# Performance work log

Hardware: AMD Instinct MI355X
Metric: run time of the kernel (lower is better)

## Reference

```python
import jax, jax.numpy as jnp
import numpy as np

N_NODES = 100000

def sage_conv(x, edge_index, Wl, bl, Wr):
    # PyG SAGEConv: out = lin_l(mean_agg(x_src -> dst)) + lin_r(x)
    src, dst = edge_index[0], edge_index[1]
    msgs = x[src]                                   # [E, F] gather
    sums = jax.ops.segment_sum(msgs, dst, num_segments=N_NODES)   # [N, F]
    cnt = jax.ops.segment_sum(jnp.ones((edge_index.shape[1],), x.dtype), dst,
                              num_segments=N_NODES)               # [N]
    mean = sums / jnp.maximum(cnt, 1.0)[:, None]
    return mean @ Wl + bl + x @ Wr


def setup_inputs() -> dict:
    key = jax.random.key(0)
    ks = jax.random.split(key, 12)
    in_dim, hid = 32, 64
    x = jax.random.normal(ks[0], (N_NODES, in_dim), dtype=jnp.float32)
    edge_index = jax.random.randint(ks[1], (2, 3200000), 0, N_NODES)
    edge_pairs = jax.random.randint(ks[2], (1000000, 2), 0, N_NODES)
    def lin(k, fi, fo):
        bound = 1.0 / np.sqrt(fi)
        return jax.random.uniform(k, (fi, fo), jnp.float32, -bound, bound)
    params = {
        'Wl1': lin(ks[3], in_dim, hid), 'bl1': jnp.zeros((hid,), jnp.float32),
        'Wr1': lin(ks[4], in_dim, hid),
        'Wl2': lin(ks[5], hid, hid),    'bl2': jnp.zeros((hid,), jnp.float32),
        'Wr2': lin(ks[6], hid, hid),
        'Wh':  lin(ks[7], 2 * hid, 1),  'bh': jnp.zeros((1,), jnp.float32),
    }
    return dict(x=x, edge_index=edge_index, edge_pairs=edge_pairs, **params)


def reference(x, edge_index, edge_pairs, Wl1, bl1, Wr1, Wl2, bl2, Wr2, Wh, bh):
    h = jax.nn.relu(sage_conv(x, edge_index, Wl1, bl1, Wr1))
    h = jax.nn.relu(sage_conv(h, edge_index, Wl2, bl2, Wr2))
    src = h[edge_pairs[:, 0]]
    dst = h[edge_pairs[:, 1]]
    edge_repr = jnp.concatenate([src, dst], axis=1)   # [P, 2*hid]
    logits = (edge_repr @ Wh + bh)[:, 0]              # [P]
    return logits
```

## Files before the change

### kernel.cpp

```cpp
#include <hip/hip_runtime.h>

typedef unsigned int uint;
typedef unsigned short ushort;
typedef __attribute__((ext_vector_type(8))) short bf16x8;
typedef __attribute__((ext_vector_type(4))) float f32x4;

#define N_NODES 100000
#define N_EDGES 3200000
#define N_PAIRS 1000000
#define N_TILES (N_NODES / 16)

#define BUCK_SHIFT 8
#define BUCK_NODES 256
#define NBUCK ((N_NODES + BUCK_NODES - 1) / BUCK_NODES)
#define CAP 8704
#define CH 8192
#define NCHB ((N_EDGES + CH - 1) / CH)

__device__ __forceinline__ float bf_lo(uint u) { return __uint_as_float(u << 16); }
__device__ __forceinline__ float bf_hi(uint u) { return __uint_as_float(u & 0xFFFF0000u); }
__device__ __forceinline__ ushort f2bf(float f) {
  uint u = __float_as_uint(f);
  return (ushort)((u + 0x7FFF + ((u >> 16) & 1)) >> 16);
}
__device__ __forceinline__ uint pack2bf(float lo, float hi) {
  return (uint)f2bf(lo) | ((uint)f2bf(hi) << 16);
}


__global__ void __launch_bounds__(256) k_prep(
    const float* __restrict__ x,
    const float* __restrict__ Wl1, const float* __restrict__ Wr1,
    const float* __restrict__ Wl2, const float* __restrict__ Wr2,
    ushort* __restrict__ xb, ushort* __restrict__ W1T, ushort* __restrict__ W2T,
    int* __restrict__ woff)
{
  int t = blockIdx.x * blockDim.x + threadIdx.x;
  if (t < N_NODES * 32) xb[t] = f2bf(x[t]);
  if (t < 4096) {
    int col = t >> 6, f = t & 63;
    float w = (f < 32) ? Wl1[f * 64 + col] : Wr1[(f - 32) * 64 + col];
    W1T[col * 64 + f] = f2bf(w);
  }
  if (t < 8192) {
    int col = t >> 7, f = t & 127;
    float w = (f < 64) ? Wl2[f * 64 + col] : Wr2[(f - 64) * 64 + col];
    W2T[col * 128 + f] = f2bf(w);
  }
  if (t < NBUCK) woff[t] = t * CAP;
}


__global__ void __launch_bounds__(256) k_binning(
    const int* __restrict__ src, const int* __restrict__ dst,
    int* __restrict__ woff, int* __restrict__ bucket_data)
{
  __shared__ int hist[NBUCK];
  __shared__ int rbase[NBUCK];
  __shared__ int roff[NBUCK];
  int t = threadIdx.x;
  int lo = blockIdx.x * CH;
  int hi = lo + CH; if (hi > N_EDGES) hi = N_EDGES;
  for (int i = t; i < NBUCK; i += 256) { hist[i] = 0; roff[i] = 0; }
  __syncthreads();
  for (int e = lo + t; e < hi; e += 256) atomicAdd(&hist[dst[e] >> BUCK_SHIFT], 1);
  __syncthreads();
  for (int i = t; i < NBUCK; i += 256)
    rbase[i] = hist[i] ? atomicAdd(&woff[i], hist[i]) : 0;
  __syncthreads();
  for (int e = lo + t; e < hi; e += 256) {
    int d = dst[e];
    int b = d >> BUCK_SHIFT;
    int r = atomicAdd(&roff[b], 1);
    int pos = rbase[b] + r;
    if (pos < (b + 1) * CAP)
      bucket_data[pos] = (src[e] << BUCK_SHIFT) | (d & (BUCK_NODES - 1));
  }
}


__global__ void __launch_bounds__(512) k_bucket_csr(
    const int* __restrict__ woff, const int* __restrict__ bucket_data,
    int* __restrict__ csr, int* __restrict__ row_beg, int* __restrict__ row_end)
{
  __shared__ int hist[BUCK_NODES];
  __shared__ int sc[BUCK_NODES];
  __shared__ int offs[BUCK_NODES];
  int b = blockIdx.x;
  int t = threadIdx.x;
  int base = b * CAP;
  int cnt = woff[b] - base;
  const int* bd = bucket_data + base;
  if (t < BUCK_NODES) hist[t] = 0;
  __syncthreads();
  for (int i = t; i < cnt; i += 512) atomicAdd(&hist[bd[i] & (BUCK_NODES - 1)], 1);
  __syncthreads();
  if (t < BUCK_NODES) sc[t] = hist[t];
  __syncthreads();
  for (int off = 1; off < BUCK_NODES; off <<= 1) {
    int u = 0;
    if (t < BUCK_NODES && t >= off) u = sc[t - off];
    __syncthreads();
    if (t < BUCK_NODES) sc[t] += u;
    __syncthreads();
  }
  if (t < BUCK_NODES) {
    int start = base + sc[t] - hist[t];
    offs[t] = start;
    int node = b * BUCK_NODES + t;
    if (node < N_NODES) { row_beg[node] = start; row_end[node] = start + hist[t]; }
  }
  __syncthreads();
  for (int i = t; i < cnt; i += 512) {
    int pv = bd[i];
    int pos = atomicAdd(&offs[pv & (BUCK_NODES - 1)], 1);
    csr[pos] = pv >> BUCK_SHIFT;
  }
}


__global__ void __launch_bounds__(256) k_gather1(
    const uint4* __restrict__ xb4, const int* __restrict__ row_beg,
    const int* __restrict__ row_end, const int* __restrict__ csr,
    uint4* __restrict__ mean1)
{
  int gid = blockIdx.x * blockDim.x + threadIdx.x;
  int n = gid >> 6;
  int lane = threadIdx.x & 63;
  if (n >= N_NODES) return;
  int slot = lane >> 2;
  int fq = lane & 3;
  int beg = row_beg[n], end = row_end[n];
  int deg = end - beg;
  float s0 = 0.f, s1 = 0.f, s2 = 0.f, s3 = 0.f, s4 = 0.f, s5 = 0.f, s6 = 0.f, s7 = 0.f;
  int i = beg;
  for (; i + 31 < end; i += 32) {
    int n0 = csr[i + slot];
    int n1 = csr[i + 16 + slot];
    uint4 a = xb4[n0 * 4 + fq];
    uint4 b = xb4[n1 * 4 + fq];
    s0 += bf_lo(a.x); s1 += bf_hi(a.x); s2 += bf_lo(a.y); s3 += bf_hi(a.y);
    s4 += bf_lo(a.z); s5 += bf_hi(a.z); s6 += bf_lo(a.w); s7 += bf_hi(a.w);
    s0 += bf_lo(b.x); s1 += bf_hi(b.x); s2 += bf_lo(b.y); s3 += bf_hi(b.y);
    s4 += bf_lo(b.z); s5 += bf_hi(b.z); s6 += bf_lo(b.w); s7 += bf_hi(b.w);
  }
  for (; i < end; i += 16) {
    if (i + slot < end) {
      uint4 a = xb4[csr[i + slot] * 4 + fq];
      s0 += bf_lo(a.x); s1 += bf_hi(a.x); s2 += bf_lo(a.y); s3 += bf_hi(a.y);
      s4 += bf_lo(a.z); s5 += bf_hi(a.z); s6 += bf_lo(a.w); s7 += bf_hi(a.w);
    }
  }
#pragma unroll
  for (int off = 4; off <= 32; off <<= 1) {
    s0 += __shfl_xor(s0, off); s1 += __shfl_xor(s1, off);
    s2 += __shfl_xor(s2, off); s3 += __shfl_xor(s3, off);
    s4 += __shfl_xor(s4, off); s5 += __shfl_xor(s5, off);
    s6 += __shfl_xor(s6, off); s7 += __shfl_xor(s7, off);
  }
  if (slot == 0) {
    float invd = (deg > 0) ? 1.f / (float)deg : 0.f;
    uint4 o;
    o.x = pack2bf(s0 * invd, s1 * invd);
    o.y = pack2bf(s2 * invd, s3 * invd);
    o.z = pack2bf(s4 * invd, s5 * invd);
    o.w = pack2bf(s6 * invd, s7 * invd);
    mean1[n * 4 + fq] = o;
  }
}

__global__ void __launch_bounds__(256) k_gather2(
    const uint4* __restrict__ hb4, const int* __restrict__ row_beg,
    const int* __restrict__ row_end, const int* __restrict__ csr,
    uint4* __restrict__ mean2)
{
  int gid = blockIdx.x * blockDim.x + threadIdx.x;
  int n = gid >> 6;
  int lane = threadIdx.x & 63;
  if (n >= N_NODES) return;
  int slot = lane >> 3;
  int fq = lane & 7;
  int beg = row_beg[n], end = row_end[n];
  int deg = end - beg;
  float s0 = 0.f, s1 = 0.f, s2 = 0.f, s3 = 0.f, s4 = 0.f, s5 = 0.f, s6 = 0.f, s7 = 0.f;
  int i = beg;
  for (; i + 31 < end; i += 32) {
    int n0 = csr[i + slot];
    int n1 = csr[i + 8 + slot];
    int n2 = csr[i + 16 + slot];
    int n3 = csr[i + 24 + slot];
    uint4 a = hb4[n0 * 8 + fq];
    uint4 b = hb4[n1 * 8 + fq];
    uint4 c = hb4[n2 * 8 + fq];
    uint4 d = hb4[n3 * 8 + fq];
    s0 += bf_lo(a.x); s1 += bf_hi(a.x); s2 += bf_lo(a.y); s3 += bf_hi(a.y);
    s4 += bf_lo(a.z); s5 += bf_hi(a.z); s6 += bf_lo(a.w); s7 += bf_hi(a.w);
    s0 += bf_lo(b.x); s1 += bf_hi(b.x); s2 += bf_lo(b.y); s3 += bf_hi(b.y);
    s4 += bf_lo(b.z); s5 += bf_hi(b.z); s6 += bf_lo(b.w); s7 += bf_hi(b.w);
    s0 += bf_lo(c.x); s1 += bf_hi(c.x); s2 += bf_lo(c.y); s3 += bf_hi(c.y);
    s4 += bf_lo(c.z); s5 += bf_hi(c.z); s6 += bf_lo(c.w); s7 += bf_hi(c.w);
    s0 += bf_lo(d.x); s1 += bf_hi(d.x); s2 += bf_lo(d.y); s3 += bf_hi(d.y);
    s4 += bf_lo(d.z); s5 += bf_hi(d.z); s6 += bf_lo(d.w); s7 += bf_hi(d.w);
  }
  for (; i < end; i += 8) {
    if (i + slot < end) {
      uint4 a = hb4[csr[i + slot] * 8 + fq];
      s0 += bf_lo(a.x); s1 += bf_hi(a.x); s2 += bf_lo(a.y); s3 += bf_hi(a.y);
      s4 += bf_lo(a.z); s5 += bf_hi(a.z); s6 += bf_lo(a.w); s7 += bf_hi(a.w);
    }
  }
#pragma unroll
  for (int off = 8; off <= 32; off <<= 1) {
    s0 += __shfl_xor(s0, off); s1 += __shfl_xor(s1, off);
    s2 += __shfl_xor(s2, off); s3 += __shfl_xor(s3, off);
    s4 += __shfl_xor(s4, off); s5 += __shfl_xor(s5, off);
    s6 += __shfl_xor(s6, off); s7 += __shfl_xor(s7, off);
  }
  if (slot == 0) {
    float invd = (deg > 0) ? 1.f / (float)deg : 0.f;
    uint4 o;
    o.x = pack2bf(s0 * invd, s1 * invd);
    o.y = pack2bf(s2 * invd, s3 * invd);
    o.z = pack2bf(s4 * invd, s5 * invd);
    o.w = pack2bf(s6 * invd, s7 * invd);
    mean2[n * 8 + fq] = o;
  }
}


__global__ void __launch_bounds__(256) k_gemm1(
    const ushort* __restrict__ mean1, const ushort* __restrict__ xb,
    const ushort* __restrict__ W1T, const float* __restrict__ bl,
    ushort* __restrict__ h1b)
{
  int wave = (blockIdx.x * blockDim.x + threadIdx.x) >> 6;
  if (wave >= N_TILES) return;
  int lane = threadIdx.x & 63;
  int lc = lane & 15;
  int lg = lane >> 4;
  int n0 = wave * 16;

  bf16x8 bfr[4][2];
#pragma unroll
  for (int j = 0; j < 4; ++j)
#pragma unroll
    for (int kk = 0; kk < 2; ++kk)
      bfr[j][kk] = *(const bf16x8*)(W1T + (j * 16 + lc) * 64 + kk * 32 + lg * 8);

  f32x4 c[4];
#pragma unroll
  for (int j = 0; j < 4; ++j) {
    float b = bl[j * 16 + lc];
    c[j][0] = b; c[j][1] = b; c[j][2] = b; c[j][3] = b;
  }

  bf16x8 a0 = *(const bf16x8*)(mean1 + (n0 + lc) * 32 + lg * 8);
  bf16x8 a1 = *(const bf16x8*)(xb    + (n0 + lc) * 32 + lg * 8);
#pragma unroll
  for (int j = 0; j < 4; ++j) {
    c[j] = __builtin_amdgcn_mfma_f32_16x16x32_bf16(a0, bfr[j][0], c[j], 0, 0, 0);
    c[j] = __builtin_amdgcn_mfma_f32_16x16x32_bf16(a1, bfr[j][1], c[j], 0, 0, 0);
  }

#pragma unroll
  for (int j = 0; j < 4; ++j)
#pragma unroll
    for (int r = 0; r < 4; ++r) {
      int node = n0 + lg * 4 + r;
      h1b[node * 64 + j * 16 + lc] = f2bf(fmaxf(c[j][r], 0.f));
    }
}

__global__ void __launch_bounds__(256) k_gemm2(
    const ushort* __restrict__ mean2, const ushort* __restrict__ h1b,
    const ushort* __restrict__ W2T, const float* __restrict__ bl,
    const float* __restrict__ Wh, float* __restrict__ u, float* __restrict__ v)
{
  int wave = (blockIdx.x * blockDim.x + threadIdx.x) >> 6;
  if (wave >= N_TILES) return;
  int lane = threadIdx.x & 63;
  int lc = lane & 15;
  int lg = lane >> 4;
  int n0 = wave * 16;

  bf16x8 bfr[4][4];
#pragma unroll
  for (int j = 0; j < 4; ++j)
#pragma unroll
    for (int kk = 0; kk < 4; ++kk)
      bfr[j][kk] = *(const bf16x8*)(W2T + (j * 16 + lc) * 128 + kk * 32 + lg * 8);

  f32x4 c[4];
#pragma unroll
  for (int j = 0; j < 4; ++j) {
    float b = bl[j * 16 + lc];
    c[j][0] = b; c[j][1] = b; c[j][2] = b; c[j][3] = b;
  }

  bf16x8 a0 = *(const bf16x8*)(mean2 + (n0 + lc) * 64 + lg * 8);
  bf16x8 a1 = *(const bf16x8*)(mean2 + (n0 + lc) * 64 + 32 + lg * 8);
  bf16x8 a2 = *(const bf16x8*)(h1b   + (n0 + lc) * 64 + lg * 8);
  bf16x8 a3 = *(const bf16x8*)(h1b   + (n0 + lc) * 64 + 32 + lg * 8);
#pragma unroll
  for (int j = 0; j < 4; ++j) {
    c[j] = __builtin_amdgcn_mfma_f32_16x16x32_bf16(a0, bfr[j][0], c[j], 0, 0, 0);
    c[j] = __builtin_amdgcn_mfma_f32_16x16x32_bf16(a1, bfr[j][1], c[j], 0, 0, 0);
    c[j] = __builtin_amdgcn_mfma_f32_16x16x32_bf16(a2, bfr[j][2], c[j], 0, 0, 0);
    c[j] = __builtin_amdgcn_mfma_f32_16x16x32_bf16(a3, bfr[j][3], c[j], 0, 0, 0);
  }

  float pu0 = 0.f, pu1 = 0.f, pu2 = 0.f, pu3 = 0.f;
  float pv0 = 0.f, pv1 = 0.f, pv2 = 0.f, pv3 = 0.f;
#pragma unroll
  for (int j = 0; j < 4; ++j) {
    float wu = Wh[j * 16 + lc];
    float wv = Wh[64 + j * 16 + lc];
    float r0 = fmaxf(c[j][0], 0.f), r1 = fmaxf(c[j][1], 0.f);
    float r2 = fmaxf(c[j][2], 0.f), r3 = fmaxf(c[j][3], 0.f);
    pu0 = fmaf(r0, wu, pu0); pv0 = fmaf(r0, wv, pv0);
    pu1 = fmaf(r1, wu, pu1); pv1 = fmaf(r1, wv, pv1);
    pu2 = fmaf(r2, wu, pu2); pv2 = fmaf(r2, wv, pv2);
    pu3 = fmaf(r3, wu, pu3); pv3 = fmaf(r3, wv, pv3);
  }
#pragma unroll
  for (int off = 1; off <= 8; off <<= 1) {
    pu0 += __shfl_xor(pu0, off); pv0 += __shfl_xor(pv0, off);
    pu1 += __shfl_xor(pu1, off); pv1 += __shfl_xor(pv1, off);
    pu2 += __shfl_xor(pu2, off); pv2 += __shfl_xor(pv2, off);
    pu3 += __shfl_xor(pu3, off); pv3 += __shfl_xor(pv3, off);
  }
  if (lc == 0) {
    int node = n0 + lg * 4;
    u[node]     = pu0; v[node]     = pv0;
    u[node + 1] = pu1; v[node + 1] = pv1;
    u[node + 2] = pu2; v[node + 2] = pv2;
    u[node + 3] = pu3; v[node + 3] = pv3;
  }
}


__global__ void __launch_bounds__(256) k_edge_lite(
    const int2* __restrict__ pairs, const float* __restrict__ u,
    const float* __restrict__ v, const float* __restrict__ bh,
    float* __restrict__ out)
{
  int e = blockIdx.x * blockDim.x + threadIdx.x;
  if (e < N_PAIRS) {
    int2 pr = pairs[e];
    out[e] = u[pr.x] + v[pr.y] + bh[0];
  }
}


extern "C" void kernel_launch(void* const* d_in, const int* in_sizes, int n_in,
                              void* d_out, int out_size, void* d_ws, size_t ws_size,
                              hipStream_t stream)
{
  const float* x   = (const float*)d_in[0];
  const int*   ei  = (const int*)d_in[1];
  const int* pairs = (const int*)d_in[2];
  const float* Wl1 = (const float*)d_in[3];
  const float* bl1 = (const float*)d_in[4];
  const float* Wr1 = (const float*)d_in[5];
  const float* Wl2 = (const float*)d_in[6];
  const float* bl2 = (const float*)d_in[7];
  const float* Wr2 = (const float*)d_in[8];
  const float* Wh  = (const float*)d_in[9];
  const float* bh  = (const float*)d_in[10];
  float* out = (float*)d_out;

  const int* src = ei;
  const int* dst = ei + N_EDGES;

  char* p = (char*)d_ws;
  auto alloc = [&](size_t bytes) {
    char* r = p;
    p += (bytes + 255) & ~(size_t)255;
    return r;
  };
  int*    woff        = (int*)alloc((size_t)NBUCK * 4);
  int*    bucket_data = (int*)alloc((size_t)NBUCK * CAP * 4);
  int*    csr         = (int*)alloc((size_t)NBUCK * CAP * 4);
  int*    row_beg     = (int*)alloc((size_t)N_NODES * 4);
  int*    row_end     = (int*)alloc((size_t)N_NODES * 4);
  ushort* xb          = (ushort*)alloc((size_t)N_NODES * 32 * 2);
  ushort* mean1       = (ushort*)alloc((size_t)N_NODES * 32 * 2);
  ushort* h1b         = (ushort*)alloc((size_t)N_NODES * 64 * 2);
  ushort* W1T         = (ushort*)alloc(64 * 64 * 2);
  ushort* W2T         = (ushort*)alloc(64 * 128 * 2);
  float*  uu          = (float*)alloc((size_t)N_NODES * 4);
  float*  vv          = (float*)alloc((size_t)N_NODES * 4);
  ushort* mean2       = (ushort*)bucket_data;

  k_prep<<<(N_NODES * 32) / 256, 256, 0, stream>>>(
      x, Wl1, Wr1, Wl2, Wr2, xb, W1T, W2T, woff);
  k_binning<<<NCHB, 256, 0, stream>>>(src, dst, woff, bucket_data);
  k_bucket_csr<<<NBUCK, 512, 0, stream>>>(woff, bucket_data, csr, row_beg, row_end);

  k_gather1<<<(N_NODES * 64) / 256, 256, 0, stream>>>(
      (const uint4*)xb, row_beg, row_end, csr, (uint4*)mean1);
  k_gemm1<<<(N_TILES * 64 + 255) / 256, 256, 0, stream>>>(mean1, xb, W1T, bl1, h1b);
  k_gather2<<<(N_NODES * 64) / 256, 256, 0, stream>>>(
      (const uint4*)h1b, row_beg, row_end, csr, (uint4*)mean2);
  k_gemm2<<<(N_TILES * 64 + 255) / 256, 256, 0, stream>>>(
      mean2, h1b, W2T, bl2, Wh, uu, vv);
  k_edge_lite<<<(N_PAIRS + 255) / 256, 256, 0, stream>>>(
      (const int2*)pairs, uu, vv, bh, out);
}
```

Baseline: 213.1 us.

## Locally sort edges in LDS before coalesced bucket writes; vectorize bf16 conversion

The binning kernel now keeps each chunk's edges in registers and builds a per-chunk bucket histogram with a wave-level prefix scan. It scatters packed entries into a shared-memory sorted buffer, then writes each bucket's run to global memory contiguously, one wave per bucket. This replaces random per-edge global scatter writes with mostly coalesced runs and avoids reading src/dst twice. Separately, the prep kernel converts x to bf16 four floats per thread with vector loads and stores. The cost is 32KB+ of LDS per block, which lowers occupancy, plus extra barriers.

```diff
diff --git a/kernel.cpp b/kernel.cpp
--- a/kernel.cpp
+++ b/kernel.cpp
@@ -16,6 +16,7 @@
 #define CAP 8704
 #define CH 8192
 #define NCHB ((N_EDGES + CH - 1) / CH)
+#define EPL (CH / 256)
 
 __device__ __forceinline__ float bf_lo(uint u) { return __uint_as_float(u << 16); }
 __device__ __forceinline__ float bf_hi(uint u) { return __uint_as_float(u & 0xFFFF0000u); }
@@ -36,7 +37,13 @@
     int* __restrict__ woff)
 {
   int t = blockIdx.x * blockDim.x + threadIdx.x;
-  if (t < N_NODES * 32) xb[t] = f2bf(x[t]);
+  if (t < N_NODES * 8) {
+    float4 f = ((const float4*)x)[t];
+    uint2 o;
+    o.x = pack2bf(f.x, f.y);
+    o.y = pack2bf(f.z, f.w);
+    ((uint2*)xb)[t] = o;
+  }
   if (t < 4096) {
     int col = t >> 6, f = t & 63;
     float w = (f < 32) ? Wl1[f * 64 + col] : Wr1[(f - 32) * 64 + col];
@@ -55,26 +62,67 @@
     const int* __restrict__ src, const int* __restrict__ dst,
     int* __restrict__ woff, int* __restrict__ bucket_data)
 {
+  __shared__ uint sorted[CH];
   __shared__ int hist[NBUCK];
+  __shared__ int pfx[NBUCK];
+  __shared__ int off[NBUCK];
   __shared__ int rbase[NBUCK];
-  __shared__ int roff[NBUCK];
   int t = threadIdx.x;
+  int w = t >> 6, lane = t & 63;
   int lo = blockIdx.x * CH;
   int hi = lo + CH; if (hi > N_EDGES) hi = N_EDGES;
-  for (int i = t; i < NBUCK; i += 256) { hist[i] = 0; roff[i] = 0; }
-  __syncthreads();
-  for (int e = lo + t; e < hi; e += 256) atomicAdd(&hist[dst[e] >> BUCK_SHIFT], 1);
-  __syncthreads();
-  for (int i = t; i < NBUCK; i += 256)
-    rbase[i] = hist[i] ? atomicAdd(&woff[i], hist[i]) : 0;
-  __syncthreads();
-  for (int e = lo + t; e < hi; e += 256) {
-    int d = dst[e];
-    int b = d >> BUCK_SHIFT;
-    int r = atomicAdd(&roff[b], 1);
-    int pos = rbase[b] + r;
-    if (pos < (b + 1) * CAP)
-      bucket_data[pos] = (src[e] << BUCK_SHIFT) | (d & (BUCK_NODES - 1));
+  for (int i = t; i < NBUCK; i += 256) hist[i] = 0;
+  __syncthreads();
+  int dreg[EPL], sreg[EPL];
+#pragma unroll
+  for (int it = 0; it < EPL; ++it) {
+    int e = lo + t + it * 256;
+    int dv = -1, sv = 0;
+    if (e < hi) { dv = dst[e]; sv = src[e]; }
+    dreg[it] = dv; sreg[it] = sv;
+    if (dv >= 0) atomicAdd(&hist[dv >> BUCK_SHIFT], 1);
+  }
+  __syncthreads();
+  if (w == 0) {
+    int carry = 0;
+    for (int c = 0; c < (NBUCK + 63) / 64; ++c) {
+      int i = c * 64 + lane;
+      int v = (i < NBUCK) ? hist[i] : 0;
+      int x = v;
+#pragma unroll
+      for (int o = 1; o < 64; o <<= 1) {
+        int y = __shfl_up(x, o);
+        if (lane >= o) x += y;
+      }
+      if (i < NBUCK) pfx[i] = carry + x - v;
+      carry += __shfl(x, 63);
+    }
+  }
+  __syncthreads();
+  for (int i = t; i < NBUCK; i += 256) {
+    off[i] = pfx[i];
+    int h = hist[i];
+    rbase[i] = h ? atomicAdd(&woff[i], h) : 0;
+  }
+  __syncthreads();
+#pragma unroll
+  for (int it = 0; it < EPL; ++it) {
+    int dv = dreg[it];
+    if (dv >= 0) {
+      int b = dv >> BUCK_SHIFT;
+      int slot = atomicAdd(&off[b], 1);
+      sorted[slot] = ((uint)sreg[it] << BUCK_SHIFT) | (uint)(dv & (BUCK_NODES - 1));
+    }
+  }
+  __syncthreads();
+  for (int b = w; b < NBUCK; b += 4) {
+    int h = hist[b];
+    int s = pfx[b];
+    int g = rbase[b];
+    int lim = (b + 1) * CAP - g;
+    if (h > lim) h = lim;
+    for (int j = lane; j < h; j += 64)
+      bucket_data[g + j] = sorted[s + j];
   }
 }
 
@@ -392,7 +440,7 @@
   float*  vv          = (float*)alloc((size_t)N_NODES * 4);
   ushort* mean2       = (ushort*)bucket_data;
 
-  k_prep<<<(N_NODES * 32) / 256, 256, 0, stream>>>(
+  k_prep<<<(N_NODES * 8 + 255) / 256, 256, 0, stream>>>(
       x, Wl1, Wr1, Wl2, Wr2, xb, W1T, W2T, woff);
   k_binning<<<NCHB, 256, 0, stream>>>(src, dst, woff, bucket_data);
   k_bucket_csr<<<NBUCK, 512, 0, stream>>>(woff, bucket_data, csr, row_beg, row_end);
```

After: 208.2 us (median of 2 runs). -2.3%, faster.
